# Performance work log

Hardware: AMD Instinct MI355X
Metric: run time of the kernel (lower is better)

## Reference

```python
import jax, jax.numpy as jnp
import numpy as np

N = 50000      # nodes
E = 800000     # edges (avg degree 16)
DIN = 128
H = 128
DOUT = 64


def setup_inputs() -> dict:
    key = jax.random.key(0)
    ks = jax.random.split(key, 8)
    x = jax.random.normal(ks[0], (N, DIN), dtype=jnp.float32)
    edge_index = jax.random.randint(ks[1], (2, E), 0, N, dtype=jnp.int32)
    def glorot(k, fi, fo):
        return jax.random.normal(k, (fi, fo), dtype=jnp.float32) * (1.0 / np.sqrt(fi))
    return {
        "x": x,
        "edge_index": edge_index,
        "W1": glorot(ks[2], DIN, H), "b1": jnp.zeros((H,), jnp.float32),
        "W2": glorot(ks[3], H, H),   "b2": jnp.zeros((H,), jnp.float32),
        "W3": glorot(ks[4], H, DOUT),"b3": jnp.zeros((DOUT,), jnp.float32),
    }


def reference(x, edge_index, W1, b1, W2, b2, W3, b3):
    n = x.shape[0]
    # GCNConv: add self-loops, symmetric degree normalization D^-1/2 (A+I) D^-1/2
    loop = jnp.arange(n, dtype=edge_index.dtype)
    src = jnp.concatenate([edge_index[0], loop])  # [E+N]
    dst = jnp.concatenate([edge_index[1], loop])
    deg = jax.ops.segment_sum(jnp.ones(src.shape, x.dtype), dst, num_segments=n)
    dinv = jnp.where(deg > 0, jax.lax.rsqrt(deg), 0.0)
    norm = dinv[src] * dinv[dst]  # [E+N]

    def conv(h, W, b):
        h = h @ W                                   # [N, out]
        msg = h[src] * norm[:, None]                # gather + scale
        return jax.ops.segment_sum(msg, dst, num_segments=n) + b

    # gelu after every layer except the last (forward breaks before act)
    h = jax.nn.gelu(conv(x, W1, b1), approximate=False)
    h = jax.nn.gelu(conv(h, W2, b2), approximate=False)
    return conv(h, W3, b3)
```

## Files before the change

### kernel.cpp

```cpp
#include <hip/hip_runtime.h>
#include <math.h>

#define NDIN 128
#define NHID 128
#define NDOUT 64

typedef _Float16 half2_t __attribute__((ext_vector_type(2)));
typedef _Float16 half4_t __attribute__((ext_vector_type(4)));
typedef _Float16 half8_t __attribute__((ext_vector_type(8)));
typedef float    float4v __attribute__((ext_vector_type(4)));

__device__ __forceinline__ float gelu_exact(float x) {
    return 0.5f * x * (1.0f + erff(x * 0.70710678118654752f));
}


__device__ void wtrans_tile(const float* __restrict__ W, _Float16* __restrict__ Wt,
                            int K, int N, int bx, int by) {
    __shared__ float tile[32][33];
    int tx = threadIdx.x & 31, ty = threadIdx.x >> 5;
    for (int i = 0; i < 32; i += 8) {
        int k = by * 32 + ty + i, nn = bx * 32 + tx;
        tile[ty + i][tx] = (k < K && nn < N) ? W[(size_t)k * N + nn] : 0.f;
    }
    __syncthreads();
    for (int i = 0; i < 32; i += 8) {
        int nn = bx * 32 + ty + i, k = by * 32 + tx;
        if (nn < N && k < K) Wt[(size_t)nn * K + k] = (_Float16)tile[tx][ty + i];
    }
}

__global__ __launch_bounds__(256) void prep0_kernel(
    const float* __restrict__ W1, _Float16* __restrict__ W1t,
    const float* __restrict__ W2, _Float16* __restrict__ W2t,
    const float* __restrict__ W3, _Float16* __restrict__ W3t,
    int* __restrict__ count, int* __restrict__ done, int n) {
    int b = blockIdx.x;
    if (b < 16) {
        wtrans_tile(W1, W1t, NDIN, NHID, b & 3, b >> 2);
    } else if (b < 32) {
        wtrans_tile(W2, W2t, NHID, NHID, (b - 16) & 3, (b - 16) >> 2);
    } else if (b < 40) {
        wtrans_tile(W3, W3t, NHID, NDOUT, (b - 32) & 1, (b - 32) >> 1);
    } else {
        int z = b - 40;
        int i = z * 256 + threadIdx.x;
        if (i < n) count[i] = 0;
        if (z == 0 && threadIdx.x < 64) done[threadIdx.x] = 0;
    }
}


__global__ void count_kernel(const int* __restrict__ dst, int* __restrict__ count, int E) {
    int e = blockIdx.x * blockDim.x + threadIdx.x;
    if (e < E) atomicAdd(&count[dst[e]], 1);
}


__global__ __launch_bounds__(256) void reduce_scan_kernel(
    const int* __restrict__ count, int* __restrict__ blocksum, int* __restrict__ blockoff,
    int* __restrict__ rowptr, float* __restrict__ dinv, int* __restrict__ done,
    int nb, int n) {
    __shared__ int s[256];
    __shared__ int flag;
    __shared__ int boff_s;
    int t = threadIdx.x;
    int i = blockIdx.x * 256 + t;
    int v = (i < n) ? count[i] : 0;
    s[t] = v;
    __syncthreads();
    for (int off = 128; off > 0; off >>= 1) {
        if (t < off) s[t] += s[t + off];
        __syncthreads();
    }
    if (t == 0) {
        atomicExch(&blocksum[blockIdx.x], s[0]);
        __threadfence();
        int old = atomicAdd(&done[0], 1);
        flag = (old == nb - 1) ? 1 : 0;
    }
    __syncthreads();
    if (flag) {
        __threadfence();
        int pv = (t < nb) ? atomicAdd(&blocksum[t], 0) : 0;
        s[t] = pv;
        __syncthreads();
        for (int off = 1; off < 256; off <<= 1) {
            int u = (t >= off) ? s[t - off] : 0;
            __syncthreads();
            s[t] += u;
            __syncthreads();
        }
        if (t < nb) atomicExch(&blockoff[t], s[t] - pv);
        if (t == 255) rowptr[n] = s[255];
        __threadfence();
        if (t == 0) atomicExch(&done[1], 1);
    } else if (t == 0) {
        while (atomicAdd(&done[1], 0) == 0) __builtin_amdgcn_s_sleep(2);
        __threadfence();
    }
    __syncthreads();
    if (t == 0) boff_s = atomicAdd(&blockoff[blockIdx.x], 0);
    s[t] = v;
    __syncthreads();
    for (int off = 1; off < 256; off <<= 1) {
        int u = (t >= off) ? s[t - off] : 0;
        __syncthreads();
        s[t] += u;
        __syncthreads();
    }
    if (i < n) {
        rowptr[i] = boff_s + s[t] - v;
        dinv[i] = rsqrtf((float)(v + 1));
    }
}


__global__ void fill_kernel(const int* __restrict__ src, const int* __restrict__ dst,
                            const float* __restrict__ dinv, const int* __restrict__ rowptr,
                            int* __restrict__ count, int2* __restrict__ adj, int E) {
    int e = blockIdx.x * blockDim.x + threadIdx.x;
    if (e >= E) return;
    int s = src[e], d = dst[e];
    int slot = atomicSub(&count[d], 1) - 1;
    int p = rowptr[d] + slot;
    adj[p] = make_int2(s, __float_as_int(dinv[s] * dinv[d]));
}


template <int BN, bool AF16>
__global__ __launch_bounds__(256) void gemm_mfma(
    const void* __restrict__ Aptr, const _Float16* __restrict__ Bt,
    _Float16* __restrict__ T, int M) {
    __shared__ _Float16 lds_a[64][136];
    __shared__ _Float16 lds_bt[BN][136];
    const int K = 128;
    int tid = threadIdx.x;
    int bm = blockIdx.x * 64;
    int wave = tid >> 6, lane = tid & 63;
    int m = lane & 15, quad = lane >> 4;

    if (AF16) {
        const _Float16* A = (const _Float16*)Aptr;
#pragma unroll
        for (int j = 0; j < 4; j++) {
            int c = tid + j * 256;
            int r = c >> 4, col = (c & 15) << 3;
            int grow = bm + r;
            uint4 v = make_uint4(0, 0, 0, 0);
            if (grow < M) v = *(const uint4*)(A + (size_t)grow * K + col);
            *(uint4*)&lds_a[r][col] = v;
        }
    } else {
        const float* A = (const float*)Aptr;
#pragma unroll
        for (int j = 0; j < 8; j++) {
            int c = tid + j * 256;
            int r = c >> 5, col = (c & 31) << 2;
            int grow = bm + r;
            float4 v = make_float4(0.f, 0.f, 0.f, 0.f);
            if (grow < M) v = *(const float4*)(A + (size_t)grow * K + col);
            half4_t h;
            h[0] = (_Float16)v.x; h[1] = (_Float16)v.y;
            h[2] = (_Float16)v.z; h[3] = (_Float16)v.w;
            *(half4_t*)&lds_a[r][col] = h;
        }
    }
    {
        const int chunks = BN * K / 8;
        for (int c = tid; c < chunks; c += 256) {
            int r = c >> 4, col = (c & 15) << 3;
            *(uint4*)&lds_bt[r][col] = *(const uint4*)(Bt + (size_t)r * K + col);
        }
    }
    __syncthreads();

    const int NT = BN / 16;
    float4v acc[NT];
#pragma unroll
    for (int nt = 0; nt < NT; nt++) acc[nt] = (float4v){0.f, 0.f, 0.f, 0.f};

    int arow = (wave << 4) + m;
#pragma unroll
    for (int kc = 0; kc < K; kc += 32) {
        half8_t a = *(const half8_t*)&lds_a[arow][kc + quad * 8];
#pragma unroll
        for (int nt = 0; nt < NT; nt++) {
            half8_t b = *(const half8_t*)&lds_bt[nt * 16 + m][kc + quad * 8];
            acc[nt] = __builtin_amdgcn_mfma_f32_16x16x32_f16(a, b, acc[nt], 0, 0, 0);
        }
    }
#pragma unroll
    for (int nt = 0; nt < NT; nt++) {
#pragma unroll
        for (int r = 0; r < 4; r++) {
            int grow = bm + (wave << 4) + (quad << 2) + r;
            if (grow < M) T[(size_t)grow * BN + nt * 16 + m] = (_Float16)acc[nt][r];
        }
    }
}


__device__ __forceinline__ half2_t agg_node128(
    const half2_t* __restrict__ t2, const int* __restrict__ rowptr,
    const int2* __restrict__ adj, const float* __restrict__ dinv,
    const float* __restrict__ bias, int node, int lane) {
    float wself = dinv[node];
    wself *= wself;
    half2_t v = t2[(size_t)node * 64 + lane];
    float accx = wself * (float)v[0], accy = wself * (float)v[1];
    int beg = rowptr[node], end = rowptr[node + 1];
    for (int e0 = beg; e0 < end; e0 += 64) {
        int rem = end - e0;
        int j = 0; float w = 0.f;
        if (lane < rem) {
            int2 ed = adj[e0 + lane];
            j = ed.x; w = __int_as_float(ed.y);
        }
        int cnt = rem < 64 ? rem : 64;
        for (int c = 0; c < cnt; c += 16) {
#pragma unroll
            for (int i = 0; i < 16; i++) {
                int jj = __builtin_amdgcn_readlane(j, c + i);
                float ww = __int_as_float(
                    __builtin_amdgcn_readlane(__float_as_int(w), c + i));
                half2_t u = t2[(size_t)jj * 64 + lane];
                accx += ww * (float)u[0];
                accy += ww * (float)u[1];
            }
        }
    }
    float2 b = ((const float2*)bias)[lane];
    accx = gelu_exact(accx + b.x);
    accy = gelu_exact(accy + b.y);
    half2_t o; o[0] = (_Float16)accx; o[1] = (_Float16)accy;
    return o;
}


template <int BN>
__global__ __launch_bounds__(256) void agg_gemm16_kernel(
    const _Float16* __restrict__ t, const int* __restrict__ rowptr,
    const int2* __restrict__ adj, const float* __restrict__ dinv,
    const float* __restrict__ bias, const _Float16* __restrict__ Bt,
    _Float16* __restrict__ T, int M) {
    __shared__ _Float16 lds_a[16][136];
    int tid = threadIdx.x;
    int wave = tid >> 6, lane = tid & 63;
    int bm = blockIdx.x * 16;
    const half2_t* t2 = (const half2_t*)t;
#pragma unroll 1
    for (int p = 0; p < 4; p++) {
        int r = (wave << 2) + p;
        int node = bm + r;
        half2_t o;
        o[0] = (_Float16)0.f; o[1] = (_Float16)0.f;
        if (node < M) o = agg_node128(t2, rowptr, adj, dinv, bias, node, lane);
        *(half2_t*)&lds_a[r][lane << 1] = o;
    }
    __syncthreads();

    int m = lane & 15, quad = lane >> 4;
    const int NT = BN / 64;
    float4v acc[NT];
#pragma unroll
    for (int nt = 0; nt < NT; nt++) acc[nt] = (float4v){0.f, 0.f, 0.f, 0.f};
#pragma unroll
    for (int kc = 0; kc < 128; kc += 32) {
        half8_t a = *(const half8_t*)&lds_a[m][kc + quad * 8];
#pragma unroll
        for (int nt = 0; nt < NT; nt++) {
            int col = wave * (BN / 4) + nt * 16 + m;
            half8_t b = *(const half8_t*)&Bt[(size_t)col * 128 + kc + quad * 8];
            acc[nt] = __builtin_amdgcn_mfma_f32_16x16x32_f16(a, b, acc[nt], 0, 0, 0);
        }
    }
#pragma unroll
    for (int nt = 0; nt < NT; nt++) {
#pragma unroll
        for (int r = 0; r < 4; r++) {
            int grow = bm + (quad << 2) + r;
            int col = wave * (BN / 4) + nt * 16 + m;
            if (grow < M) T[(size_t)grow * BN + col] = (_Float16)acc[nt][r];
        }
    }
}


template <int F, bool DOGELU, bool OUTF16>
__global__ __launch_bounds__(256) void agg_kernel(
    const _Float16* __restrict__ t, const int* __restrict__ rowptr,
    const int2* __restrict__ adj, const float* __restrict__ dinv,
    const float* __restrict__ bias, void* __restrict__ outp, int n) {
    int node = (int)((blockIdx.x * blockDim.x + threadIdx.x) >> 6);
    int lane = threadIdx.x & 63;
    if (node >= n) return;

    float wself = dinv[node];
    wself *= wself;
    int beg = rowptr[node];
    int end = rowptr[node + 1];

    if (F == 128) {
        const half2_t* t2 = (const half2_t*)t;
        half2_t v = t2[(size_t)node * 64 + lane];
        float accx = wself * (float)v[0], accy = wself * (float)v[1];
        for (int e0 = beg; e0 < end; e0 += 64) {
            int rem = end - e0;
            int j = 0; float w = 0.f;
            if (lane < rem) {
                int2 ed = adj[e0 + lane];
                j = ed.x; w = __int_as_float(ed.y);
            }
            int cnt = rem < 64 ? rem : 64;
            for (int c = 0; c < cnt; c += 16) {
#pragma unroll
                for (int i = 0; i < 16; i++) {
                    int jj = __builtin_amdgcn_readlane(j, c + i);
                    float ww = __int_as_float(
                        __builtin_amdgcn_readlane(__float_as_int(w), c + i));
                    half2_t u = t2[(size_t)jj * 64 + lane];
                    accx += ww * (float)u[0];
                    accy += ww * (float)u[1];
                }
            }
        }
        float2 b = ((const float2*)bias)[lane];
        accx += b.x; accy += b.y;
        if (DOGELU) { accx = gelu_exact(accx); accy = gelu_exact(accy); }
        if (OUTF16) {
            half2_t o; o[0] = (_Float16)accx; o[1] = (_Float16)accy;
            ((half2_t*)outp)[(size_t)node * 64 + lane] = o;
        } else {
            float2 o; o.x = accx; o.y = accy;
            ((float2*)outp)[(size_t)node * 64 + lane] = o;
        }
    } else {
        float acc = wself * (float)t[(size_t)node * 64 + lane];
        for (int e0 = beg; e0 < end; e0 += 64) {
            int rem = end - e0;
            int j = 0; float w = 0.f;
            if (lane < rem) {
                int2 ed = adj[e0 + lane];
                j = ed.x; w = __int_as_float(ed.y);
            }
            int cnt = rem < 64 ? rem : 64;
            for (int c = 0; c < cnt; c += 16) {
#pragma unroll
                for (int i = 0; i < 16; i++) {
                    int jj = __builtin_amdgcn_readlane(j, c + i);
                    float ww = __int_as_float(
                        __builtin_amdgcn_readlane(__float_as_int(w), c + i));
                    acc += ww * (float)t[(size_t)jj * 64 + lane];
                }
            }
        }
        acc += bias[lane];
        if (DOGELU) acc = gelu_exact(acc);
        if (OUTF16) ((_Float16*)outp)[(size_t)node * 64 + lane] = (_Float16)acc;
        else        ((float*)outp)[(size_t)node * 64 + lane] = acc;
    }
}


extern "C" void kernel_launch(void* const* d_in, const int* in_sizes, int n_in,
                              void* d_out, int out_size, void* d_ws, size_t ws_size,
                              hipStream_t stream) {
    const float* x  = (const float*)d_in[0];
    const int* edge = (const int*)d_in[1];
    const float* W1 = (const float*)d_in[2];
    const float* b1 = (const float*)d_in[3];
    const float* W2 = (const float*)d_in[4];
    const float* b2 = (const float*)d_in[5];
    const float* W3 = (const float*)d_in[6];
    const float* b3 = (const float*)d_in[7];
    float* out = (float*)d_out;

    const int N = in_sizes[0] / NDIN;
    const int E = in_sizes[1] / 2;
    const int* src = edge;
    const int* dst = edge + E;
    const int NB = (N + 255) / 256;

    char* p = (char*)d_ws;
    auto alloc = [&](size_t bytes) {
        char* q = p;
        p += (bytes + 255) & ~(size_t)255;
        return q;
    };
    int*       count    = (int*)alloc((size_t)N * 4);
    int*       rowptr   = (int*)alloc((size_t)(N + 1) * 4);
    int*       blocksum = (int*)alloc((size_t)NB * 4);
    int*       blockoff = (int*)alloc((size_t)NB * 4);
    int*       done     = (int*)alloc(256);
    float*     dinv     = (float*)alloc((size_t)N * 4);
    int2*      adj      = (int2*)alloc((size_t)E * 8);
    _Float16*  W1t      = (_Float16*)alloc((size_t)NHID * NDIN * 2);
    _Float16*  W2t      = (_Float16*)alloc((size_t)NHID * NHID * 2);
    _Float16*  W3t      = (_Float16*)alloc((size_t)NDOUT * NHID * 2);
    _Float16*  tbuf     = (_Float16*)alloc((size_t)N * NHID * 2);
    _Float16*  hbuf     = (_Float16*)alloc((size_t)N * NHID * 2);

    dim3 blk(256);
    int mtiles = (N + 63) / 64;
    int ntiles16 = (N + 15) / 16;
    int eblocks = (E + 255) / 256;
    int agg_blocks = (N + 3) / 4;

    prep0_kernel<<<40 + NB, blk, 0, stream>>>(W1, W1t, W2, W2t, W3, W3t, count, done, N);
    count_kernel<<<eblocks, blk, 0, stream>>>(dst, count, E);
    reduce_scan_kernel<<<NB, blk, 0, stream>>>(count, blocksum, blockoff, rowptr,
                                               dinv, done, NB, N);
    fill_kernel<<<eblocks, blk, 0, stream>>>(src, dst, dinv, rowptr, count, adj, E);
    gemm_mfma<128, false><<<mtiles, blk, 0, stream>>>(x, W1t, tbuf, N);
    agg_gemm16_kernel<128><<<ntiles16, blk, 0, stream>>>(tbuf, rowptr, adj, dinv, b1,
                                                         W2t, hbuf, N);
    agg_gemm16_kernel<64><<<ntiles16, blk, 0, stream>>>(hbuf, rowptr, adj, dinv, b2,
                                                        W3t, tbuf, N);
    agg_kernel<64, false, false><<<agg_blocks, blk, 0, stream>>>(tbuf, rowptr, adj,
                                                                 dinv, b3, out, N);
}
```

Before: 289.5 us.

## Fuse edge counting with first GEMM and scan with CSR fill

Merges the degree-count kernel with the layer-1 GEMM into one launch, recording each edge's atomic slot so the fill no longer needs a second atomic pass. The scan and fill are merged into one 1024-thread kernel that uses a grid-wide spin barrier before scattering edges, computing the normalisation from the counts directly. The GEMM now reads W1t from global memory instead of staging it in LDS. This removes two launches and the atomicSub pass, at the cost of a persistent-grid barrier that depends on all scan blocks being resident at once, plus an extra eslot buffer.

```diff
diff --git a/kernel.cpp b/kernel.cpp
--- a/kernel.cpp
+++ b/kernel.cpp
@@ -51,26 +51,85 @@
 }
 
 
-__global__ void count_kernel(const int* __restrict__ dst, int* __restrict__ count, int E) {
-    int e = blockIdx.x * blockDim.x + threadIdx.x;
-    if (e < E) atomicAdd(&count[dst[e]], 1);
-}
-
-
-__global__ __launch_bounds__(256) void reduce_scan_kernel(
+template <int BN>
+__device__ __forceinline__ void gemm_phaseB(
+    const _Float16 (*lds_a)[136], const _Float16* __restrict__ Bt,
+    _Float16* __restrict__ T, int bm, int M) {
+    int tid = threadIdx.x;
+    int wave = tid >> 6, lane = tid & 63;
+    int m = lane & 15, quad = lane >> 4;
+    const int NT = BN / 16;
+    float4v acc[NT];
+#pragma unroll
+    for (int nt = 0; nt < NT; nt++) acc[nt] = (float4v){0.f, 0.f, 0.f, 0.f};
+    int arow = (wave << 4) + m;
+#pragma unroll
+    for (int kc = 0; kc < 128; kc += 32) {
+        half8_t a = *(const half8_t*)&lds_a[arow][kc + quad * 8];
+#pragma unroll
+        for (int nt = 0; nt < NT; nt++) {
+            half8_t b = *(const half8_t*)&Bt[(size_t)(nt * 16 + m) * 128 + kc + quad * 8];
+            acc[nt] = __builtin_amdgcn_mfma_f32_16x16x32_f16(a, b, acc[nt], 0, 0, 0);
+        }
+    }
+#pragma unroll
+    for (int nt = 0; nt < NT; nt++) {
+#pragma unroll
+        for (int r = 0; r < 4; r++) {
+            int grow = bm + (wave << 4) + (quad << 2) + r;
+            if (grow < M) T[(size_t)grow * BN + nt * 16 + m] = (_Float16)acc[nt][r];
+        }
+    }
+}
+
+
+__global__ __launch_bounds__(256) void count_gemm1_kernel(
+    const int* __restrict__ dst, int* __restrict__ count, int* __restrict__ eslot, int E,
+    const float* __restrict__ x, const _Float16* __restrict__ W1t,
+    _Float16* __restrict__ T, int M, int cblocks) {
+    __shared__ _Float16 lds_a[64][136];
+    int b = blockIdx.x;
+    if (b < cblocks) {
+        int e = b * 256 + threadIdx.x;
+        if (e < E) eslot[e] = atomicAdd(&count[dst[e]], 1);
+        return;
+    }
+    int bm = (b - cblocks) * 64;
+    int tid = threadIdx.x;
+#pragma unroll
+    for (int j = 0; j < 8; j++) {
+        int c = tid + j * 256;
+        int r = c >> 5, col = (c & 31) << 2;
+        int grow = bm + r;
+        float4 v = make_float4(0.f, 0.f, 0.f, 0.f);
+        if (grow < M) v = *(const float4*)(x + (size_t)grow * 128 + col);
+        half4_t h;
+        h[0] = (_Float16)v.x; h[1] = (_Float16)v.y;
+        h[2] = (_Float16)v.z; h[3] = (_Float16)v.w;
+        *(half4_t*)&lds_a[r][col] = h;
+    }
+    __syncthreads();
+    gemm_phaseB<128>(lds_a, W1t, T, bm, M);
+}
+
+
+__global__ __launch_bounds__(1024) void scan_fill_kernel(
     const int* __restrict__ count, int* __restrict__ blocksum, int* __restrict__ blockoff,
     int* __restrict__ rowptr, float* __restrict__ dinv, int* __restrict__ done,
-    int nb, int n) {
+    const int* __restrict__ src, const int* __restrict__ dst,
+    const int* __restrict__ eslot, int2* __restrict__ adj,
+    int nb, int n, int E) {
     __shared__ int s[256];
     __shared__ int flag;
     __shared__ int boff_s;
     int t = threadIdx.x;
+    bool sc = t < 256;
     int i = blockIdx.x * 256 + t;
-    int v = (i < n) ? count[i] : 0;
-    s[t] = v;
+    int v = 0;
+    if (sc) { v = (i < n) ? count[i] : 0; s[t] = v; }
     __syncthreads();
     for (int off = 128; off > 0; off >>= 1) {
-        if (t < off) s[t] += s[t + off];
+        if (sc && t < off) s[t] += s[t + off];
         __syncthreads();
     }
     if (t == 0) {
@@ -82,16 +141,16 @@
     __syncthreads();
     if (flag) {
         __threadfence();
-        int pv = (t < nb) ? atomicAdd(&blocksum[t], 0) : 0;
-        s[t] = pv;
+        int pv = 0;
+        if (sc) { pv = (t < nb) ? atomicAdd(&blocksum[t], 0) : 0; s[t] = pv; }
         __syncthreads();
         for (int off = 1; off < 256; off <<= 1) {
-            int u = (t >= off) ? s[t - off] : 0;
+            int u = (sc && t >= off) ? s[t - off] : 0;
             __syncthreads();
-            s[t] += u;
+            if (sc) s[t] += u;
             __syncthreads();
         }
-        if (t < nb) atomicExch(&blockoff[t], s[t] - pv);
+        if (sc && t < nb) atomicExch(&blockoff[t], s[t] - pv);
         if (t == 255) rowptr[n] = s[255];
         __threadfence();
         if (t == 0) atomicExch(&done[1], 1);
@@ -101,102 +160,32 @@
     }
     __syncthreads();
     if (t == 0) boff_s = atomicAdd(&blockoff[blockIdx.x], 0);
-    s[t] = v;
+    if (sc) s[t] = v;
     __syncthreads();
     for (int off = 1; off < 256; off <<= 1) {
-        int u = (t >= off) ? s[t - off] : 0;
+        int u = (sc && t >= off) ? s[t - off] : 0;
         __syncthreads();
-        s[t] += u;
+        if (sc) s[t] += u;
         __syncthreads();
     }
-    if (i < n) {
+    if (sc && i < n) {
         rowptr[i] = boff_s + s[t] - v;
         dinv[i] = rsqrtf((float)(v + 1));
     }
-}
-
-
-__global__ void fill_kernel(const int* __restrict__ src, const int* __restrict__ dst,
-                            const float* __restrict__ dinv, const int* __restrict__ rowptr,
-                            int* __restrict__ count, int2* __restrict__ adj, int E) {
-    int e = blockIdx.x * blockDim.x + threadIdx.x;
-    if (e >= E) return;
-    int s = src[e], d = dst[e];
-    int slot = atomicSub(&count[d], 1) - 1;
-    int p = rowptr[d] + slot;
-    adj[p] = make_int2(s, __float_as_int(dinv[s] * dinv[d]));
-}
-
-
-template <int BN, bool AF16>
-__global__ __launch_bounds__(256) void gemm_mfma(
-    const void* __restrict__ Aptr, const _Float16* __restrict__ Bt,
-    _Float16* __restrict__ T, int M) {
-    __shared__ _Float16 lds_a[64][136];
-    __shared__ _Float16 lds_bt[BN][136];
-    const int K = 128;
-    int tid = threadIdx.x;
-    int bm = blockIdx.x * 64;
-    int wave = tid >> 6, lane = tid & 63;
-    int m = lane & 15, quad = lane >> 4;
-
-    if (AF16) {
-        const _Float16* A = (const _Float16*)Aptr;
-#pragma unroll
-        for (int j = 0; j < 4; j++) {
-            int c = tid + j * 256;
-            int r = c >> 4, col = (c & 15) << 3;
-            int grow = bm + r;
-            uint4 v = make_uint4(0, 0, 0, 0);
-            if (grow < M) v = *(const uint4*)(A + (size_t)grow * K + col);
-            *(uint4*)&lds_a[r][col] = v;
-        }
-    } else {
-        const float* A = (const float*)Aptr;
-#pragma unroll
-        for (int j = 0; j < 8; j++) {
-            int c = tid + j * 256;
-            int r = c >> 5, col = (c & 31) << 2;
-            int grow = bm + r;
-            float4 v = make_float4(0.f, 0.f, 0.f, 0.f);
-            if (grow < M) v = *(const float4*)(A + (size_t)grow * K + col);
-            half4_t h;
-            h[0] = (_Float16)v.x; h[1] = (_Float16)v.y;
-            h[2] = (_Float16)v.z; h[3] = (_Float16)v.w;
-            *(half4_t*)&lds_a[r][col] = h;
-        }
-    }
-    {
-        const int chunks = BN * K / 8;
-        for (int c = tid; c < chunks; c += 256) {
-            int r = c >> 4, col = (c & 15) << 3;
-            *(uint4*)&lds_bt[r][col] = *(const uint4*)(Bt + (size_t)r * K + col);
-        }
-    }
-    __syncthreads();
-
-    const int NT = BN / 16;
-    float4v acc[NT];
-#pragma unroll
-    for (int nt = 0; nt < NT; nt++) acc[nt] = (float4v){0.f, 0.f, 0.f, 0.f};
-
-    int arow = (wave << 4) + m;
-#pragma unroll
-    for (int kc = 0; kc < K; kc += 32) {
-        half8_t a = *(const half8_t*)&lds_a[arow][kc + quad * 8];
-#pragma unroll
-        for (int nt = 0; nt < NT; nt++) {
-            half8_t b = *(const half8_t*)&lds_bt[nt * 16 + m][kc + quad * 8];
-            acc[nt] = __builtin_amdgcn_mfma_f32_16x16x32_f16(a, b, acc[nt], 0, 0, 0);
-        }
-    }
-#pragma unroll
-    for (int nt = 0; nt < NT; nt++) {
-#pragma unroll
-        for (int r = 0; r < 4; r++) {
-            int grow = bm + (wave << 4) + (quad << 2) + r;
-            if (grow < M) T[(size_t)grow * BN + nt * 16 + m] = (_Float16)acc[nt][r];
-        }
+    __threadfence();
+    __syncthreads();
+    if (t == 0) {
+        atomicAdd(&done[2], 1);
+        while (atomicAdd(&done[2], 0) < nb) __builtin_amdgcn_s_sleep(2);
+    }
+    __syncthreads();
+    int stride = nb * 1024;
+    for (int e = blockIdx.x * 1024 + t; e < E; e += stride) {
+        int ss = src[e], d = dst[e];
+        int base = __hip_atomic_load(&rowptr[d], __ATOMIC_RELAXED,
+                                     __HIP_MEMORY_SCOPE_AGENT);
+        float wv = rsqrtf((float)(count[ss] + 1)) * rsqrtf((float)(count[d] + 1));
+        adj[base + eslot[e]] = make_int2(ss, __float_as_int(wv));
     }
 }
 
@@ -394,6 +383,7 @@
     int*       blockoff = (int*)alloc((size_t)NB * 4);
     int*       done     = (int*)alloc(256);
     float*     dinv     = (float*)alloc((size_t)N * 4);
+    int*       eslot    = (int*)alloc((size_t)E * 4);
     int2*      adj      = (int2*)alloc((size_t)E * 8);
     _Float16*  W1t      = (_Float16*)alloc((size_t)NHID * NDIN * 2);
     _Float16*  W2t      = (_Float16*)alloc((size_t)NHID * NHID * 2);
@@ -402,17 +392,17 @@
     _Float16*  hbuf     = (_Float16*)alloc((size_t)N * NHID * 2);
 
     dim3 blk(256);
+    dim3 blk1k(1024);
     int mtiles = (N + 63) / 64;
     int ntiles16 = (N + 15) / 16;
     int eblocks = (E + 255) / 256;
     int agg_blocks = (N + 3) / 4;
 
     prep0_kernel<<<40 + NB, blk, 0, stream>>>(W1, W1t, W2, W2t, W3, W3t, count, done, N);
-    count_kernel<<<eblocks, blk, 0, stream>>>(dst, count, E);
-    reduce_scan_kernel<<<NB, blk, 0, stream>>>(count, blocksum, blockoff, rowptr,
-                                               dinv, done, NB, N);
-    fill_kernel<<<eblocks, blk, 0, stream>>>(src, dst, dinv, rowptr, count, adj, E);
-    gemm_mfma<128, false><<<mtiles, blk, 0, stream>>>(x, W1t, tbuf, N);
+    count_gemm1_kernel<<<eblocks + mtiles, blk, 0, stream>>>(
+        dst, count, eslot, E, x, W1t, tbuf, N, eblocks);
+    scan_fill_kernel<<<NB, blk1k, 0, stream>>>(count, blocksum, blockoff, rowptr, dinv,
+                                               done, src, dst, eslot, adj, NB, N, E);
     agg_gemm16_kernel<128><<<ntiles16, blk, 0, stream>>>(tbuf, rowptr, adj, dinv, b1,
                                                          W2t, hbuf, N);
     agg_gemm16_kernel<64><<<ntiles16, blk, 0, stream>>>(hbuf, rowptr, adj, dinv, b2,
```

After: 332.4 us. 14.8% more time.

## Replicate degree counters and record per-edge slots to remove fill-stage atomics

Applied to the files above, without the earlier changes.

Degree counting now spreads atomics over eight replicated counter arrays, chosen by block index, and records each edge's returned slot. The scan kernel turns the replicas into per-replica prefix offsets, so the fill kernel computes each edge's CSR position directly instead of doing a second atomicSub pass. The first GEMM is moved before the scan. This adds an E-sized slot buffer, an 8x larger counter array to zero and read, and extra memory traffic in exchange for less atomic contention and no atomics in fill.

```diff
diff --git a/kernel.cpp b/kernel.cpp
--- a/kernel.cpp
+++ b/kernel.cpp
@@ -4,6 +4,7 @@
 #define NDIN 128
 #define NHID 128
 #define NDOUT 64
+#define NREP 8
 
 typedef _Float16 half2_t __attribute__((ext_vector_type(2)));
 typedef _Float16 half4_t __attribute__((ext_vector_type(4)));
@@ -34,7 +35,7 @@
     const float* __restrict__ W1, _Float16* __restrict__ W1t,
     const float* __restrict__ W2, _Float16* __restrict__ W2t,
     const float* __restrict__ W3, _Float16* __restrict__ W3t,
-    int* __restrict__ count, int* __restrict__ done, int n) {
+    int* __restrict__ countR, int* __restrict__ done, int n) {
     int b = blockIdx.x;
     if (b < 16) {
         wtrans_tile(W1, W1t, NDIN, NHID, b & 3, b >> 2);
@@ -45,20 +46,22 @@
     } else {
         int z = b - 40;
         int i = z * 256 + threadIdx.x;
-        if (i < n) count[i] = 0;
+        if (i < NREP * n) countR[i] = 0;
         if (z == 0 && threadIdx.x < 64) done[threadIdx.x] = 0;
     }
 }
 
 
-__global__ void count_kernel(const int* __restrict__ dst, int* __restrict__ count, int E) {
-    int e = blockIdx.x * blockDim.x + threadIdx.x;
-    if (e < E) atomicAdd(&count[dst[e]], 1);
+__global__ void count_kernel(const int* __restrict__ dst, int* __restrict__ countR,
+                             int* __restrict__ eslot, int E, int n) {
+    int b = blockIdx.x;
+    int e = b * 256 + threadIdx.x;
+    if (e < E) eslot[e] = atomicAdd(&countR[(b & (NREP - 1)) * n + dst[e]], 1);
 }
 
 
 __global__ __launch_bounds__(256) void reduce_scan_kernel(
-    const int* __restrict__ count, int* __restrict__ blocksum, int* __restrict__ blockoff,
+    int* __restrict__ countR, int* __restrict__ blocksum, int* __restrict__ blockoff,
     int* __restrict__ rowptr, float* __restrict__ dinv, int* __restrict__ done,
     int nb, int n) {
     __shared__ int s[256];
@@ -66,8 +69,18 @@
     __shared__ int boff_s;
     int t = threadIdx.x;
     int i = blockIdx.x * 256 + t;
-    int v = (i < n) ? count[i] : 0;
-    s[t] = v;
+    int deg = 0;
+    if (i < n) {
+        int pre = 0;
+#pragma unroll
+        for (int r = 0; r < NREP; r++) {
+            int c = countR[r * n + i];
+            countR[r * n + i] = pre;
+            pre += c;
+        }
+        deg = pre;
+    }
+    s[t] = deg;
     __syncthreads();
     for (int off = 128; off > 0; off >>= 1) {
         if (t < off) s[t] += s[t + off];
@@ -101,7 +114,7 @@
     }
     __syncthreads();
     if (t == 0) boff_s = atomicAdd(&blockoff[blockIdx.x], 0);
-    s[t] = v;
+    s[t] = deg;
     __syncthreads();
     for (int off = 1; off < 256; off <<= 1) {
         int u = (t >= off) ? s[t - off] : 0;
@@ -110,20 +123,21 @@
         __syncthreads();
     }
     if (i < n) {
-        rowptr[i] = boff_s + s[t] - v;
-        dinv[i] = rsqrtf((float)(v + 1));
+        rowptr[i] = boff_s + s[t] - deg;
+        dinv[i] = rsqrtf((float)(deg + 1));
     }
 }
 
 
 __global__ void fill_kernel(const int* __restrict__ src, const int* __restrict__ dst,
-                            const float* __restrict__ dinv, const int* __restrict__ rowptr,
-                            int* __restrict__ count, int2* __restrict__ adj, int E) {
-    int e = blockIdx.x * blockDim.x + threadIdx.x;
+                            const int* __restrict__ eslot, const float* __restrict__ dinv,
+                            const int* __restrict__ rowptr, const int* __restrict__ countR,
+                            int2* __restrict__ adj, int E, int n) {
+    int e = blockIdx.x * 256 + threadIdx.x;
     if (e >= E) return;
     int s = src[e], d = dst[e];
-    int slot = atomicSub(&count[d], 1) - 1;
-    int p = rowptr[d] + slot;
+    int r = (e >> 8) & (NREP - 1);
+    int p = rowptr[d] + countR[r * n + d] + eslot[e];
     adj[p] = make_int2(s, __float_as_int(dinv[s] * dinv[d]));
 }
 
@@ -381,6 +395,7 @@
     const int* src = edge;
     const int* dst = edge + E;
     const int NB = (N + 255) / 256;
+    const int NBZ = (NREP * N + 255) / 256;
 
     char* p = (char*)d_ws;
     auto alloc = [&](size_t bytes) {
@@ -388,12 +403,13 @@
         p += (bytes + 255) & ~(size_t)255;
         return q;
     };
-    int*       count    = (int*)alloc((size_t)N * 4);
+    int*       countR   = (int*)alloc((size_t)NREP * N * 4);
     int*       rowptr   = (int*)alloc((size_t)(N + 1) * 4);
     int*       blocksum = (int*)alloc((size_t)NB * 4);
     int*       blockoff = (int*)alloc((size_t)NB * 4);
     int*       done     = (int*)alloc(256);
     float*     dinv     = (float*)alloc((size_t)N * 4);
+    int*       eslot    = (int*)alloc((size_t)E * 4);
     int2*      adj      = (int2*)alloc((size_t)E * 8);
     _Float16*  W1t      = (_Float16*)alloc((size_t)NHID * NDIN * 2);
     _Float16*  W2t      = (_Float16*)alloc((size_t)NHID * NHID * 2);
@@ -407,12 +423,14 @@
     int eblocks = (E + 255) / 256;
     int agg_blocks = (N + 3) / 4;
 
-    prep0_kernel<<<40 + NB, blk, 0, stream>>>(W1, W1t, W2, W2t, W3, W3t, count, done, N);
-    count_kernel<<<eblocks, blk, 0, stream>>>(dst, count, E);
-    reduce_scan_kernel<<<NB, blk, 0, stream>>>(count, blocksum, blockoff, rowptr,
+    prep0_kernel<<<40 + NBZ, blk, 0, stream>>>(W1, W1t, W2, W2t, W3, W3t,
+                                               countR, done, N);
+    count_kernel<<<eblocks, blk, 0, stream>>>(dst, countR, eslot, E, N);
+    gemm_mfma<128, false><<<mtiles, blk, 0, stream>>>(x, W1t, tbuf, N);
+    reduce_scan_kernel<<<NB, blk, 0, stream>>>(countR, blocksum, blockoff, rowptr,
                                                dinv, done, NB, N);
-    fill_kernel<<<eblocks, blk, 0, stream>>>(src, dst, dinv, rowptr, count, adj, E);
-    gemm_mfma<128, false><<<mtiles, blk, 0, stream>>>(x, W1t, tbuf, N);
+    fill_kernel<<<eblocks, blk, 0, stream>>>(src, dst, eslot, dinv, rowptr, countR,
+                                             adj, E, N);
     agg_gemm16_kernel<128><<<ntiles16, blk, 0, stream>>>(tbuf, rowptr, adj, dinv, b1,
                                                          W2t, hbuf, N);
     agg_gemm16_kernel<64><<<ntiles16, blk, 0, stream>>>(hbuf, rowptr, adj, dinv, b2,
```

After: 269.0 us. 1.08x faster.
